# Performance work log

Hardware: AMD Instinct MI355X
Metric: run time of the kernel (lower is better)

The kernel has to match this reference:

```python
import jax, jax.numpy as jnp
import numpy as np

B, CIN, COUT, K, H, W, WDIM = 16, 512, 512, 3, 64, 64, 512


def setup_inputs() -> dict:
    key = jax.random.key(0)
    k1, k2, k3, k4 = jax.random.split(key, 4)
    x = jax.random.normal(k1, (B, CIN, H, W), dtype=jnp.float32)
    w = jax.random.normal(k2, (B, WDIM), dtype=jnp.float32)
    # Equalized-LR init: init_std = 1/lrmul = 1.0 -> unit normal weights
    conv_w = jax.random.normal(k3, (K, K, CIN, COUT), dtype=jnp.float32)
    mod_w = jax.random.normal(k4, (WDIM, CIN), dtype=jnp.float32)
    mod_b = jnp.zeros((CIN,), dtype=jnp.float32)
    return {"x": x, "w": w, "conv_w": conv_w, "mod_w": mod_w, "mod_b": mod_b}


def reference(x, w, conv_w, mod_w, mod_b):
    # runtime coefficients (gain=1, lrmul=1): he_std = gain/sqrt(fan_in)
    coef_conv = np.float32(1.0 / np.sqrt(K * K * CIN))
    coef_mod = np.float32(1.0 / np.sqrt(WDIM))

    # style modulation: Dense + Bias + 1.0  -> [B, CIN]
    style = w @ (coef_mod * mod_w) + mod_b + 1.0

    # per-sample modulated weight [B, K, K, CIN, COUT]
    weight = (coef_conv * conv_w)[None] * style[:, None, None, :, None]

    # demodulate: rsqrt of sum of squares over (K, K, CIN) per output channel
    d = jax.lax.rsqrt(jnp.sum(jnp.square(weight), axis=(1, 2, 3)) + 1e-8)  # [B, COUT]
    weight = weight * d[:, None, None, None, :]

    # grouped conv via batch->channel-group reshape (StyleGAN2 trick)
    wg = jnp.transpose(weight, (1, 2, 3, 0, 4)).reshape(K, K, CIN, B * COUT)
    xg = x.reshape(1, B * CIN, H, W)
    y = jax.lax.conv_general_dilated(
        xg, wg, window_strides=(1, 1), padding="SAME",
        dimension_numbers=("NCHW", "HWIO", "NCHW"),
        feature_group_count=B,
    )
    return y.reshape(B, COUT, H, W)
```

## Files before the change

kernel.cpp:

```cpp
#include <hip/hip_runtime.h>
#include <hip/hip_bf16.h>

#define NB    16
#define CIN   512
#define COUT  512
#define HH    64
#define WW    64
#define HWSZ  4096
#define WDIMN 512

typedef __attribute__((ext_vector_type(8))) short bf16x8;
typedef __attribute__((ext_vector_type(4))) float f32x4;

__device__ __forceinline__ unsigned short f2bf(float f) {
    unsigned int u = __float_as_uint(f);
    unsigned int lsb = (u >> 16) & 1u;
    u += 0x7fffu + lsb;
    return (unsigned short)(u >> 16);
}

__device__ __forceinline__ void gload_lds16(const void* g, void* l) {
    __builtin_amdgcn_global_load_lds(
        (const __attribute__((address_space(1))) unsigned char*)g,
        (__attribute__((address_space(3))) unsigned char*)l,
        16, 0, 0);
}

__global__ void k_style(const float* __restrict__ w, const float* __restrict__ mod_w,
                        const float* __restrict__ mod_b, float* __restrict__ style) {
    const int b = blockIdx.x, t = threadIdx.x;
    __shared__ float wl[WDIMN];
    wl[t] = w[b * WDIMN + t];
    wl[t + 256] = w[b * WDIMN + t + 256];
    __syncthreads();
    float a0 = 0.f, a1 = 0.f;
    const int c0 = t, c1 = t + 256;
    for (int j = 0; j < WDIMN; ++j) {
        const float wj = wl[j];
        a0 += wj * mod_w[j * CIN + c0];
        a1 += wj * mod_w[j * CIN + c1];
    }
    const float coef = 0.044194173824159216f;
    style[b * CIN + c0] = coef * a0 + mod_b[c0] + 1.0f;
    style[b * CIN + c1] = coef * a1 + mod_b[c1] + 1.0f;
}

__global__ void k_s2(const float* __restrict__ cw, float* __restrict__ s2) {
    const int i = blockIdx.x * 256 + threadIdx.x;
    float a = 0.f;
#pragma unroll
    for (int tap = 0; tap < 9; ++tap) {
        const float v = cw[tap * (CIN * COUT) + i];
        a += v * v;
    }
    s2[i] = a;
}

__global__ void k_demod(const float* __restrict__ style, const float* __restrict__ s2,
                        float* __restrict__ dd) {
    const int b = blockIdx.x, t = threadIdx.x;
    __shared__ float st2[CIN];
    {
        const float s0 = style[b * CIN + t], s1 = style[b * CIN + t + 256];
        st2[t] = s0 * s0;
        st2[t + 256] = s1 * s1;
    }
    __syncthreads();
    float a0 = 0.f, a1 = 0.f;
    for (int ci = 0; ci < CIN; ++ci) {
        const float sv = st2[ci];
        a0 += sv * s2[ci * COUT + t];
        a1 += sv * s2[ci * COUT + t + 256];
    }
    const float c2 = 1.0f / 4608.0f;
    dd[b * COUT + t] = rsqrtf(c2 * a0 + 1e-8f);
    dd[b * COUT + t + 256] = rsqrtf(c2 * a1 + 1e-8f);
}

__global__ void k_wmod(const float* __restrict__ cw, const float* __restrict__ style,
                       const float* __restrict__ dd, unsigned short* __restrict__ wmod,
                       int b_start, int gcount) {
    const int tap = blockIdx.x;
    const int co0 = blockIdx.y * 64;
    const int ci0 = blockIdx.z * 128;
    const int t = threadIdx.x;

    __shared__ float tile[128][65];
    __shared__ float sst[16 * 128];
    {
        const int j = t & 63, isub = t >> 6;
        for (int i = isub; i < 128; i += 4)
            tile[i][j] = cw[(size_t)tap * CIN * COUT + (size_t)(ci0 + i) * COUT + co0 + j];
    }
    for (int i = t; i < gcount * 128; i += 256)
        sst[i] = style[(b_start + (i >> 7)) * CIN + ci0 + (i & 127)];
    __syncthreads();

    const float coef = 0.014731391274719736f;
    const int cq = t & 31;
    const int rsub = t >> 5;
    const int totrows = gcount * 64;
    for (int g = rsub; g < totrows; g += 8) {
        const int bbl = g >> 6;
        const int co_r = g & 63;
        const int bg = b_start + bbl;
        const float dv = dd[bg * COUT + co0 + co_r] * coef;
        const float v0 = tile[4 * cq + 0][co_r] * sst[bbl * 128 + 4 * cq + 0] * dv;
        const float v1 = tile[4 * cq + 1][co_r] * sst[bbl * 128 + 4 * cq + 1] * dv;
        const float v2 = tile[4 * cq + 2][co_r] * sst[bbl * 128 + 4 * cq + 2] * dv;
        const float v3 = tile[4 * cq + 3][co_r] * sst[bbl * 128 + 4 * cq + 3] * dv;
        uint2 pk;
        pk.x = (unsigned int)f2bf(v0) | ((unsigned int)f2bf(v1) << 16);
        pk.y = (unsigned int)f2bf(v2) | ((unsigned int)f2bf(v3) << 16);
        *(uint2*)&wmod[((size_t)(bbl * 9 + tap) * COUT + co0 + co_r) * CIN + ci0 + 4 * cq] = pk;
    }
}

__global__ void k_xt(const float* __restrict__ x, unsigned short* __restrict__ xT, int b_start) {
    const int bbl = blockIdx.x;
    const int b = b_start + bbl;
    const int hw0 = blockIdx.y * 64;
    const int ci0 = blockIdx.z * 64;
    const int t = threadIdx.x;

    __shared__ float tile[64][65];
    {
        const int j = t & 63, isub = t >> 6;
        for (int i = isub; i < 64; i += 4)
            tile[i][j] = x[((size_t)b * CIN + ci0 + i) * HWSZ + hw0 + j];
    }
    __syncthreads();

    const int cq = t & 15;
    const int rs = t >> 4;
    for (int r = rs; r < 64; r += 16) {
        const float v0 = tile[4 * cq + 0][r];
        const float v1 = tile[4 * cq + 1][r];
        const float v2 = tile[4 * cq + 2][r];
        const float v3 = tile[4 * cq + 3][r];
        uint2 pk;
        pk.x = (unsigned int)f2bf(v0) | ((unsigned int)f2bf(v1) << 16);
        pk.y = (unsigned int)f2bf(v2) | ((unsigned int)f2bf(v3) << 16);
        *(uint2*)&xT[((size_t)bbl * HWSZ + hw0 + r) * CIN + ci0 + 4 * cq] = pk;
    }
}

__global__ __launch_bounds__(256, 2)
void k_conv(const unsigned short* __restrict__ xT, const unsigned short* __restrict__ wmod,
            float* __restrict__ out, int b_start, int gcount) {
    int st, ct, bbl;
    {
        const int id = blockIdx.x;
        if (gcount == 16) {
            const int xcd = id & 7;
            const int slot = id >> 3;
            bbl = xcd + 8 * (slot >> 7);
            const int rem = slot & 127;
            ct = rem >> 5;
            st = rem & 31;
        } else {
            st = id & 31; ct = (id >> 5) & 3; bbl = id >> 7;
        }
    }
    const int b = b_start + bbl;
    const int r0 = st * 2;
    const int co0 = ct * 128;

    const int t = threadIdx.x;
    const int lane = t & 63;
    const int wid = t >> 6;
    const int wrow = wid >> 1;
    const int wcol = wid & 1;

    __shared__ __align__(16) unsigned char smem[4 * 66 * 128 + 2 * 128 * 128];
    unsigned char* Xs = smem;
    unsigned char* As = smem + 4 * 66 * 128;

    const f32x4 fzero = {0.f, 0.f, 0.f, 0.f};

    if (t < 64) {
        const int s = t >> 3;
        const int row = s >> 1, col = (s & 1) ? 65 : 0;
        *(f32x4*)(Xs + (row * 66 + col) * 128 + (t & 7) * 16) = fzero;
    }
    if (r0 == 0) {
        for (int idx = t; idx < 66 * 8; idx += 256)
            *(f32x4*)(Xs + (idx >> 3) * 128 + (idx & 7) * 16) = fzero;
    }
    if (r0 == 62) {
        for (int idx = t; idx < 66 * 8; idx += 256)
            *(f32x4*)(Xs + (3 * 66 + (idx >> 3)) * 128 + (idx & 7) * 16) = fzero;
    }

    f32x4 acc[4][4];
#pragma unroll
    for (int i = 0; i < 4; ++i)
#pragma unroll
        for (int j = 0; j < 4; ++j) acc[i][j] = fzero;

    const size_t xTbase = (size_t)bbl * HWSZ * CIN;

    auto stageA = [&](int tap, int bsel, int ci0) {
        const unsigned short* gb = wmod + ((size_t)(bbl * 9 + tap) * COUT + co0) * CIN + ci0;
        unsigned char* dbase = As + bsel * 16384;
#pragma unroll
        for (int i = 0; i < 4; ++i) {
            const int la = wid + 4 * i;
            const int row = la * 8 + (lane >> 3);
            const int kb = ((lane & 7) * 16) ^ ((row & 7) << 4);
            gload_lds16((const unsigned char*)(gb + (size_t)row * CIN) + kb,
                        dbase + la * 1024);
        }
    };

    int buf = 0;
    for (int cc = 0; cc < 8; ++cc) {
        const int ci0 = cc * 64;

#pragma unroll
        for (int i = 0; i < 8; ++i) {
            const int li = wid + 4 * i;
            const int row = li >> 3;
            const int c0 = 1 + (li & 7) * 8;
            const int ih = r0 - 1 + row;
            if (ih >= 0 && ih < HH) {
                const int col = c0 + (lane >> 3);
                const int pxidx = row * 66 + col;
                const int kb = ((lane & 7) * 16) ^ ((pxidx & 7) << 4);
                const int iw = col - 1;
                gload_lds16((const unsigned char*)(xT + xTbase + (size_t)(ih * WW + iw) * CIN + ci0) + kb,
                            Xs + (row * 66 + c0) * 128);
            }
        }

        stageA(0, buf, ci0);
        __syncthreads();

        for (int tap = 0; tap < 9; ++tap) {
            if (tap < 8) stageA(tap + 1, buf ^ 1, ci0);
            const int dh = tap / 3 - 1, dw = tap % 3 - 1;
            const unsigned char* Ab = As + buf * 16384;
#pragma unroll
            for (int k32 = 0; k32 < 2; ++k32) {
                bf16x8 af[4], bfv[4];
#pragma unroll
                for (int ma = 0; ma < 4; ++ma) {
                    const int co_r = wrow * 64 + ma * 16 + (lane & 15);
                    const int kb = (k32 * 64 + (lane >> 4) * 16) ^ ((co_r & 7) << 4);
                    af[ma] = *(const bf16x8*)(Ab + co_r * 128 + kb);
                }
#pragma unroll
                for (int nb = 0; nb < 4; ++nb) {
                    const int px = wcol * 64 + nb * 16 + (lane & 15);
                    const int trow = (px >> 6) + 1 + dh;
                    const int tcol = (px & 63) + 1 + dw;
                    const int pxidx = trow * 66 + tcol;
                    const int kb = (k32 * 64 + (lane >> 4) * 16) ^ ((pxidx & 7) << 4);
                    bfv[nb] = *(const bf16x8*)(Xs + pxidx * 128 + kb);
                }
#pragma unroll
                for (int ma = 0; ma < 4; ++ma)
#pragma unroll
                    for (int nb = 0; nb < 4; ++nb)
                        acc[ma][nb] = __builtin_amdgcn_mfma_f32_16x16x32_bf16(
                            af[ma], bfv[nb], acc[ma][nb], 0, 0, 0);
            }
            __syncthreads();
            buf ^= 1;
        }
    }

#pragma unroll
    for (int ma = 0; ma < 4; ++ma) {
        const int co = co0 + wrow * 64 + ma * 16 + ((lane >> 4) << 2);
#pragma unroll
        for (int nb = 0; nb < 4; ++nb) {
            const int px = wcol * 64 + nb * 16 + (lane & 15);
            const int oh = r0 + (px >> 6);
            const int ow = px & 63;
            float* o = out + (((size_t)b * COUT + co) * HH + oh) * WW + ow;
#pragma unroll
            for (int jj = 0; jj < 4; ++jj) o[(size_t)jj * HWSZ] = acc[ma][nb][jj];
        }
    }
}

extern "C" void kernel_launch(void* const* d_in, const int* in_sizes, int n_in,
                              void* d_out, int out_size, void* d_ws, size_t ws_size,
                              hipStream_t stream) {
    (void)in_sizes; (void)n_in; (void)out_size;
    const float* x     = (const float*)d_in[0];
    const float* w     = (const float*)d_in[1];
    const float* convw = (const float*)d_in[2];
    const float* mod_w = (const float*)d_in[3];
    const float* mod_b = (const float*)d_in[4];
    float* out = (float*)d_out;

    unsigned char* ws = (unsigned char*)d_ws;
    const size_t OFF_STYLE = 0;
    const size_t OFF_S2 = 32768;
    const size_t OFF_D = OFF_S2 + 1048576;
    const size_t OFF_BIG = OFF_D + 32768;
    const size_t PER_B_W = (size_t)9 * COUT * CIN * 2;
    const size_t PER_B_X = (size_t)HWSZ * CIN * 2;
    const size_t PER_B = PER_B_W + PER_B_X;

    if (ws_size < OFF_BIG + PER_B) return;
    const size_t avail = ws_size - OFF_BIG;
    const int G = (avail >= 16 * PER_B) ? 16 : (avail >= 4 * PER_B ? 4 : 1);

    float* style = (float*)(ws + OFF_STYLE);
    float* s2    = (float*)(ws + OFF_S2);
    float* dd    = (float*)(ws + OFF_D);
    unsigned short* wmod = (unsigned short*)(ws + OFF_BIG);
    unsigned short* xT   = (unsigned short*)(ws + OFF_BIG + (size_t)G * PER_B_W);

    k_style<<<dim3(16), dim3(256), 0, stream>>>(w, mod_w, mod_b, style);
    k_s2<<<dim3(1024), dim3(256), 0, stream>>>(convw, s2);
    k_demod<<<dim3(16), dim3(256), 0, stream>>>(style, s2, dd);

    for (int b0 = 0; b0 < NB; b0 += G) {
        k_wmod<<<dim3(9, 8, 4), dim3(256), 0, stream>>>(convw, style, dd, wmod, b0, G);
        k_xt<<<dim3(G, 64, 8), dim3(256), 0, stream>>>(x, xT, b0);
        k_conv<<<dim3(32 * 4 * G), dim3(256), 0, stream>>>(xT, wmod, out, b0, G);
    }
}
```

Before: 406.9 us.

## Flatten tap/channel loop into prefetch-two weight pipeline with manual waitcnts

Restructures the main loop so the modulated-weight tile for step g+2 is issued while step g computes. __syncthreads is replaced by explicit s_waitcnt vmcnt/lgkmcnt and s_barrier, so outstanding loads can stay in flight across the barrier. The next input-channel chunk of X is also staged at the end of the last tap. This aims to hide global-to-LDS latency that was previously exposed at every tap boundary. It risks race hazards: X is overwritten in place with only two A buffers, and the vmcnt accounting depends on lanes that skip loads for padded rows.

```diff
diff --git a/kernel.cpp b/kernel.cpp
--- a/kernel.cpp
+++ b/kernel.cpp
@@ -200,9 +200,10 @@
 
     const size_t xTbase = (size_t)bbl * HWSZ * CIN;
 
-    auto stageA = [&](int tap, int bsel, int ci0) {
-        const unsigned short* gb = wmod + ((size_t)(bbl * 9 + tap) * COUT + co0) * CIN + ci0;
-        unsigned char* dbase = As + bsel * 16384;
+    auto stageA = [&](int gidx) {
+        const int tap2 = gidx % 9, cc2 = gidx / 9;
+        const unsigned short* gb = wmod + ((size_t)(bbl * 9 + tap2) * COUT + co0) * CIN + cc2 * 64;
+        unsigned char* dbase = As + (gidx & 1) * 16384;
 #pragma unroll
         for (int i = 0; i < 4; ++i) {
             const int la = wid + 4 * i;
@@ -212,11 +213,8 @@
                         dbase + la * 1024);
         }
     };
-
-    int buf = 0;
-    for (int cc = 0; cc < 8; ++cc) {
-        const int ci0 = cc * 64;
-
+    auto stageX = [&](int ccn) {
+        const int ci0 = ccn * 64;
 #pragma unroll
         for (int i = 0; i < 8; ++i) {
             const int li = wid + 4 * i;
@@ -227,19 +225,25 @@
                 const int col = c0 + (lane >> 3);
                 const int pxidx = row * 66 + col;
                 const int kb = ((lane & 7) * 16) ^ ((pxidx & 7) << 4);
-                const int iw = col - 1;
-                gload_lds16((const unsigned char*)(xT + xTbase + (size_t)(ih * WW + iw) * CIN + ci0) + kb,
+                gload_lds16((const unsigned char*)(xT + xTbase + (size_t)(ih * WW + col - 1) * CIN + ci0) + kb,
                             Xs + (row * 66 + c0) * 128);
             }
         }
-
-        stageA(0, buf, ci0);
-        __syncthreads();
-
+    };
+
+    stageX(0);
+    stageA(0);
+    stageA(1);
+    asm volatile("s_waitcnt vmcnt(4) lgkmcnt(0)" ::: "memory");
+    __builtin_amdgcn_s_barrier();
+
+    for (int cc = 0; cc < 8; ++cc) {
+#pragma unroll
         for (int tap = 0; tap < 9; ++tap) {
-            if (tap < 8) stageA(tap + 1, buf ^ 1, ci0);
+            const int g = cc * 9 + tap;
+            const unsigned char* Ab = As + (g & 1) * 16384;
             const int dh = tap / 3 - 1, dw = tap % 3 - 1;
-            const unsigned char* Ab = As + buf * 16384;
+
 #pragma unroll
             for (int k32 = 0; k32 < 2; ++k32) {
                 bf16x8 af[4], bfv[4];
@@ -265,8 +269,16 @@
                         acc[ma][nb] = __builtin_amdgcn_mfma_f32_16x16x32_bf16(
                             af[ma], bfv[nb], acc[ma][nb], 0, 0, 0);
             }
-            __syncthreads();
-            buf ^= 1;
+
+            asm volatile("s_waitcnt lgkmcnt(0)" ::: "memory");
+            __builtin_amdgcn_s_barrier();
+
+            if (tap == 8 && cc < 7) stageX(cc + 1);
+            if (g < 70) stageA(g + 2);
+
+            if (g == 70) asm volatile("s_waitcnt vmcnt(0)" ::: "memory");
+            else         asm volatile("s_waitcnt vmcnt(4)" ::: "memory");
+            __builtin_amdgcn_s_barrier();
         }
     }
 
```

Result: faster. 391.5 us (-3.8%).
